# Kernel tuning notes

Hardware: AMD Instinct MI355X
Metric: run time of the kernel (lower is better)

Reference implementation:

```python
import jax, jax.numpy as jnp
import numpy as np
from functools import partial

B, C, FD, H, W = 8, 256, 128, 64, 64
POSC = 34  # 32 learned pos channels + 2 raw meshgrid channels


def create_meshgrid(h, w):
    # kornia-style normalized grid in [-1, 1], returned as [1, 2, h, w] (x, y)
    xs = jnp.linspace(-1.0, 1.0, w, dtype=jnp.float32)
    ys = jnp.linspace(-1.0, 1.0, h, dtype=jnp.float32)
    gy, gx = jnp.meshgrid(ys, xs, indexing='ij')
    return jnp.stack([gx, gy], axis=0)[None]  # [1,2,h,w]


def conv1x1(x, w, b):
    return jnp.einsum('bchw,oc->bohw', x, w) + b[None, :, None, None]


def pos_gen(feat, pg_w1, pg_b1, pg_w2, pg_b2):
    # PosGen type=2 with detach: two 1x1 'mul' layers (conv + ReLU, no norm)
    b, c, h, w = feat.shape
    feat = jax.lax.stop_gradient(feat)
    pos = jnp.broadcast_to(create_meshgrid(h, w), (b, 2, h, w))
    inp = jnp.concatenate([pos + 1.0, feat], axis=1)           # [b, feat_dim+2, h, w]
    h1 = jax.nn.relu(conv1x1(inp, pg_w1, pg_b1))               # [b, feat_dim, h, w]
    h2 = jax.nn.relu(conv1x1(h1, pg_w2, pg_b2))                # [b, 32, h, w]
    return jnp.concatenate([h2, pos], axis=1)                  # [b, 34, h, w]


def fuser(x, feat, w1, b1, w2, b2):
    # fuser_1D: concat along channels, 1x1 -> hidden (ReLU) -> 1x1 -> 256
    z = jnp.concatenate([x, feat], axis=1)
    z = jax.nn.relu(conv1x1(z, w1, b1))
    return conv1x1(z, w2, b2)


def conv_y(y, dw_w, dw_b, pw_w, pw_b):
    # BasicDWLayer: depthwise 3x3 + pointwise 1x1, no norm, no activation
    z = jax.lax.conv_general_dilated(
        y, dw_w, window_strides=(1, 1), padding='SAME',
        feature_group_count=y.shape[1],
        dimension_numbers=('NCHW', 'OIHW', 'NCHW')) + dw_b[None, :, None, None]
    return conv1x1(z, pw_w, pw_b)


def matching_forward(x, y, feat1, feat2,
                     pg_w1, pg_b1, pg_w2, pg_b2,
                     fus_w1, fus_b1, fus_w2, fus_b2,
                     dw_w, dw_b, pw_w, pw_b,
                     dustbin_vec, dustbin_pos):
    b, c, hx, wx = x.shape
    hy, wy = y.shape[2], y.shape[3]

    posf = pos_gen(feat2, pg_w1, pg_b1, pg_w2, pg_b2)          # [b, 34, hy, wy]
    c_pose = posf.shape[1]
    pos = posf.reshape(b, 1, c_pose, hy * wy).swapaxes(-1, -2)  # [b,1,Nk,34]

    xf = fuser(x, feat1, fus_w1, fus_b1, fus_w2, fus_b2)
    yf = fuser(y, feat2, fus_w1, fus_b1, fus_w2, fus_b2)
    yf = conv_y(yf, dw_w, dw_b, pw_w, pw_b)
    d = yf.shape[1]

    q = xf.reshape(b, 1, d, hx * wx).swapaxes(-1, -2)           # [b,1,Nq,256]
    k = yf.reshape(b, 1, d, hy * wy).swapaxes(-1, -2)           # [b,1,Nk,256]

    # dustbin token augmentation
    k = jnp.concatenate([k, jnp.broadcast_to(dustbin_vec, (b, 1, 1, d))], axis=-2)
    pos = jnp.concatenate([pos, jnp.broadcast_to(dustbin_pos, (b, 1, 1, c_pose))], axis=-2)

    # single-head cross-attention: values are the positional channels
    scores = jnp.einsum('bhqc,bhkc->bhqk', q, k) / jnp.sqrt(jnp.float32(d))
    attn = jax.nn.softmax(scores, axis=-1)
    out = jnp.einsum('bhqk,bhkd->bhqd', attn, pos)              # [b,1,Nq,34]
    return out.swapaxes(-1, -2).reshape(b, c_pose, hx, wx)


def setup_inputs() -> dict:
    key = jax.random.key(0)
    ks = jax.random.split(key, 20)
    s = 0.05
    return {
        'x': jax.random.normal(ks[0], (B, C, H, W), jnp.float32),
        'y': jax.random.normal(ks[1], (B, C, H, W), jnp.float32),
        'feat1': jax.random.normal(ks[2], (B, FD, H, W), jnp.float32),
        'feat2': jax.random.normal(ks[3], (B, FD, H, W), jnp.float32),
        # PosGen type-2 mapping: (feat_dim+2)->feat_dim, feat_dim->(hidden-2=32)
        'pg_w1': jax.random.normal(ks[4], (FD, FD + 2), jnp.float32) * s,
        'pg_b1': jnp.zeros((FD,), jnp.float32),
        'pg_w2': jax.random.normal(ks[5], (32, FD), jnp.float32) * s,
        'pg_b2': jnp.zeros((32,), jnp.float32),
        # fuser_1D: (256+128)->256 hidden, hidden->256
        'fus_w1': jax.random.normal(ks[6], (256, C + FD), jnp.float32) * s,
        'fus_b1': jnp.zeros((256,), jnp.float32),
        'fus_w2': jax.random.normal(ks[7], (C, 256), jnp.float32) * s,
        'fus_b2': jnp.zeros((C,), jnp.float32),
        # conv_y: depthwise 3x3 + pointwise 1x1
        'dw_w': jax.random.normal(ks[8], (C, 1, 3, 3), jnp.float32) * s,
        'dw_b': jnp.zeros((C,), jnp.float32),
        'pw_w': jax.random.normal(ks[9], (C, C), jnp.float32) * s,
        'pw_b': jnp.zeros((C,), jnp.float32),
        'dustbin_vec': jax.random.uniform(ks[10], (1, 1, 1, C), jnp.float32) / 10.0,
        'dustbin_pos': jnp.zeros((1, 1, 1, POSC), jnp.float32) - 10.0,
    }


def reference(x, y, feat1, feat2,
              pg_w1, pg_b1, pg_w2, pg_b2,
              fus_w1, fus_b1, fus_w2, fus_b2,
              dw_w, dw_b, pw_w, pw_b,
              dustbin_vec, dustbin_pos):
    return matching_forward(x, y, feat1, feat2,
                            pg_w1, pg_b1, pg_w2, pg_b2,
                            fus_w1, fus_b1, fus_w2, fus_b2,
                            dw_w, dw_b, pw_w, pw_b,
                            dustbin_vec, dustbin_pos)
```

## Files before the change

### kernel.cpp

```cpp
#include <hip/hip_runtime.h>
#include <hip/hip_bf16.h>

typedef __hip_bfloat16 bf16;
typedef unsigned short ushort_t;
typedef __bf16 bf16x8 __attribute__((ext_vector_type(8)));
typedef float  f32x4  __attribute__((ext_vector_type(4)));

#define HW    4096
#define NB    8
#define KSTR  4160
#define NTOK  32768
#define PROWS 64
#define QSCALE 0.0901684400557f

__device__ __forceinline__ float lde(const void* p, size_t i, int f32f) {
    return f32f ? ((const float*)p)[i] : (float)((const bf16*)p)[i];
}
__device__ __forceinline__ ushort_t f2bu(float f){ union { __bf16 b; ushort_t u; } cv; cv.b = (__bf16)f; return cv.u; }

__device__ __forceinline__ void async_cp16(const void* g, void* l) {
    __builtin_amdgcn_global_load_lds(
        (const __attribute__((address_space(1))) unsigned int*)g,
        (__attribute__((address_space(3))) unsigned int*)l, 16, 0, 0);
}

__global__ void detect_kernel(const ushort_t* xb, int* flag)
{
    __shared__ int cnt;
    const int t = threadIdx.x;
    if (t == 0) cnt = 0;
    __syncthreads();
    ushort_t h = xb[2*t];
    int e = (h >> 7) & 0xFF;
    if (e >= 133) atomicAdd(&cnt, 1);
    __syncthreads();
    if (t == 0) *flag = (cnt > 8) ? 1 : 0;
}

struct WsPtrs {
    bf16 *fw1t, *fw2t, *pwt, *pgw1t, *pgw2t, *dwt, *pos;
    float *posw, *fb1, *fb2, *pwb, *pgb1, *pgb2, *dwb;
};

__global__ __launch_bounds__(256) void prep_kernel(
    const void* fus_w1, const void* fus_w2, const void* pw_w,
    const void* pg_w1, const void* pg_w2, const void* dw_w,
    const void* fus_b1, const void* fus_b2, const void* pw_b,
    const void* pg_b1, const void* pg_b2, const void* dw_b,
    const void* dpos, WsPtrs W, const int* flag)
{
    const int f = *flag;
    const long n_w1 = 98304, n_w2 = 65536, n_pw = 65536, n_g1 = 16384, n_g2 = 4096;
    const long n_posw = 256, n_dwt = 2304;
    const long n_b = 256, n_gb1 = 128, n_gb2 = 32;
    const long n_mesh = 65536;
    const long n_pad  = 8L*14*KSTR;
    const long n_dust = 272;
    const long n_zt   = 8L*34*63;
    const long total = n_w1+n_w2+n_pw+n_g1+n_g2+n_posw+n_dwt
                     + 3*n_b + n_gb1 + n_gb2 + n_b + n_mesh + n_pad + n_dust + n_zt;

    for (long i = blockIdx.x*256L + threadIdx.x; i < total; i += gridDim.x*256L) {
        long j = i;
        if (j < n_w1) { W.fw1t[j] = __float2bfloat16(lde(fus_w1, j, f)); continue; } j -= n_w1;
        if (j < n_w2) { W.fw2t[j] = __float2bfloat16(lde(fus_w2, j, f)); continue; } j -= n_w2;
        if (j < n_pw) { W.pwt[j]  = __float2bfloat16(lde(pw_w,  j, f)); continue; } j -= n_pw;
        if (j < n_g1) { W.pgw1t[j] = __float2bfloat16(lde(pg_w1, (j>>7)*130 + 2 + (j&127), f)); continue; } j -= n_g1;
        if (j < n_g2) { W.pgw2t[j] = __float2bfloat16(lde(pg_w2, j, f)); continue; } j -= n_g2;
        if (j < n_posw) { W.posw[j] = lde(pg_w1, (j>>1)*130 + (j&1), f); continue; } j -= n_posw;
        if (j < n_dwt) { W.dwt[j] = __float2bfloat16(lde(dw_w, (j&255)*9 + (j>>8), f)); continue; } j -= n_dwt;
        if (j < n_b)   { W.fb1[j] = lde(fus_b1, j, f); continue; } j -= n_b;
        if (j < n_b)   { W.fb2[j] = lde(fus_b2, j, f); continue; } j -= n_b;
        if (j < n_b)   { W.pwb[j] = lde(pw_b, j, f); continue; } j -= n_b;
        if (j < n_gb1) { W.pgb1[j] = lde(pg_b1, j, f); continue; } j -= n_gb1;
        if (j < n_gb2) { W.pgb2[j] = lde(pg_b2, j, f); continue; } j -= n_gb2;
        if (j < n_b)   { W.dwb[j] = lde(dw_b, j, f); continue; } j -= n_b;
        if (j < n_mesh) {
            long b = j >> 13; int rr = (int)((j>>12)&1); int tok = (int)(j & 4095);
            float v = rr ? (-1.f + 2.f*(float)((tok>>6)&63)/63.f)
                         : (-1.f + 2.f*(float)(tok&63)/63.f);
            W.pos[((size_t)b*PROWS + 32 + rr)*KSTR + tok] = __float2bfloat16(v);
            continue;
        } j -= n_mesh;
        if (j < n_pad) {
            long b = j / (14L*KSTR); long rem = j % (14L*KSTR);
            int row = 34 + (int)(rem / KSTR); int tok = (int)(rem % KSTR);
            W.pos[((size_t)b*PROWS + row)*KSTR + tok] = __float2bfloat16(row == 34 ? 1.f : 0.f);
            continue;
        } j -= n_pad;
        if (j < n_dust) {
            long b = j / 34; int ch = (int)(j % 34);
            W.pos[((size_t)b*PROWS + ch)*KSTR + 4096] = __float2bfloat16(lde(dpos, ch, f));
            continue;
        } j -= n_dust;
        { long b = j / (34*63); long rem = j % (34*63);
          int ch = (int)(rem / 63); int cc = (int)(rem % 63);
          W.pos[((size_t)b*PROWS + ch)*KSTR + 4097 + cc] = __float2bfloat16(0.f); }
    }
}

__global__ __launch_bounds__(256) void transpose_kernel(
    const void* main_src, const void* feat_src, bf16* __restrict__ dst, const int* flag)
{
    __shared__ float Tt[64*65];
    const int t = threadIdx.x;
    const int p0 = blockIdx.x * 64;
    const int cht = blockIdx.y;
    const int b = blockIdx.z;
    const int f = *flag;

    const void* src; int ch0, srcC, dc0;
    if (cht < 4) { src = main_src; ch0 = cht*64; srcC = 256; dc0 = ch0; }
    else         { src = feat_src; ch0 = (cht-4)*64; srcC = 128; dc0 = 256 + (cht-4)*64; }

    const int p = t & 63, cq = t >> 6;
    #pragma unroll
    for (int e = 0; e < 16; ++e) {
        int c = e*4 + cq;
        Tt[p*65 + c] = lde(src, ((size_t)b*srcC + ch0 + c)*HW + p0 + p, f);
    }
    __syncthreads();
    const int pr = t >> 2, cs = (t & 3) * 16;
    union { uint4 u4[2]; ushort_t us[16]; } pk;
    #pragma unroll
    for (int u = 0; u < 16; ++u) pk.us[u] = f2bu(Tt[pr*65 + cs + u]);
    ushort_t* op = (ushort_t*)dst + ((size_t)b*HW + p0 + pr)*384 + dc0 + cs;
    *(uint4*)op = pk.u4[0];
    *((uint4*)op + 1) = pk.u4[1];
}

template<int MT, bool RELU, bool POSEPI, int OMODE>
__global__ __launch_bounds__(256) void gemm_mfma(
    const bf16* __restrict__ A, int sa,
    const bf16* __restrict__ Bw, int ldb,
    const float* __restrict__ bias, const float* __restrict__ posw,
    bf16* __restrict__ out, int sm, int K, float oscale)
{
    const int t = threadIdx.x;
    const int w = t >> 6, lane = t & 63;
    const int n = lane & 15, quad = lane >> 4;
    const int p0 = blockIdx.x * 128;
    const int m0 = blockIdx.y * (MT*16);
    const int rowbase = p0 + w*32;

    f32x4 acc[2][MT];
    #pragma unroll
    for (int pt = 0; pt < 2; ++pt)
        #pragma unroll
        for (int mt = 0; mt < MT; ++mt) acc[pt][mt] = (f32x4){0.f,0.f,0.f,0.f};

    for (int k0 = 0; k0 < K; k0 += 32) {
        bf16x8 ap[2];
        #pragma unroll
        for (int pt = 0; pt < 2; ++pt)
            ap[pt] = *(const bf16x8*)&A[(size_t)(rowbase + pt*16 + n)*sa + k0 + quad*8];
        #pragma unroll
        for (int mt = 0; mt < MT; ++mt) {
            bf16x8 bw = *(const bf16x8*)&Bw[(size_t)(m0 + mt*16 + n)*ldb + k0 + quad*8];
            acc[0][mt] = __builtin_amdgcn_mfma_f32_16x16x32_bf16(ap[0], bw, acc[0][mt], 0, 0, 0);
            acc[1][mt] = __builtin_amdgcn_mfma_f32_16x16x32_bf16(ap[1], bw, acc[1][mt], 0, 0, 0);
        }
    }

    #pragma unroll
    for (int mt = 0; mt < MT; ++mt) {
        const int m = m0 + mt*16 + n;
        const float bi = bias[m];
        float w0 = 0.f, w1 = 0.f;
        if (POSEPI) { w0 = posw[m*2]; w1 = posw[m*2 + 1]; }
        #pragma unroll
        for (int pt = 0; pt < 2; ++pt) {
            const int tokb = rowbase + pt*16 + quad*4;
            if (OMODE == 1) {
                union { uint2 u2; ushort_t us[4]; } pk;
                #pragma unroll
                for (int r = 0; r < 4; ++r) {
                    float v = acc[pt][mt][r] + bi;
                    if (RELU) v = fmaxf(v, 0.f);
                    pk.us[r] = f2bu(v * oscale);
                }
                size_t oi = ((size_t)(tokb >> 12)*PROWS + m)*KSTR + (tokb & 4095);
                *(uint2*)((ushort_t*)out + oi) = pk.u2;
            } else {
                #pragma unroll
                for (int r = 0; r < 4; ++r) {
                    int tok = tokb + r;
                    float v = acc[pt][mt][r] + bi;
                    if (POSEPI) {
                        float gx1 = 2.f * (float)(tok & 63) / 63.f;
                        float gy1 = 2.f * (float)((tok >> 6) & 63) / 63.f;
                        v += w0*gx1 + w1*gy1;
                    }
                    if (RELU) v = fmaxf(v, 0.f);
                    v *= oscale;
                    size_t row = (OMODE == 2) ? (size_t)tok + 64*(size_t)(tok >> 12) : (size_t)tok;
                    out[row*sm + m] = __float2bfloat16(v);
                }
            }
        }
    }
}

__global__ __launch_bounds__(256) void dw_kernel(
    const bf16* __restrict__ in, const bf16* __restrict__ dwt,
    const float* __restrict__ dwb, bf16* __restrict__ out)
{
    const int t = threadIdx.x;
    const int tok = blockIdx.x*8 + (t >> 5);
    const int c8 = (t & 31) * 8;
    const int b = tok >> 12, p = tok & 4095;
    const int i = p >> 6, j = p & 63;

    float acc[8];
    #pragma unroll
    for (int u = 0; u < 8; ++u) acc[u] = dwb[c8 + u];

    #pragma unroll
    for (int di = 0; di < 3; ++di) {
        int ii = i + di - 1;
        if (ii < 0 || ii >= 64) continue;
        #pragma unroll
        for (int dj = 0; dj < 3; ++dj) {
            int jj = j + dj - 1;
            if (jj < 0 || jj >= 64) continue;
            int tok2 = (b << 12) + ii*64 + jj;
            bf16x8 xv = *(const bf16x8*)&in[(size_t)tok2*256 + c8];
            bf16x8 wv = *(const bf16x8*)&dwt[(di*3 + dj)*256 + c8];
            #pragma unroll
            for (int u = 0; u < 8; ++u) acc[u] += (float)xv[u] * (float)wv[u];
        }
    }
    union { uint4 u4; ushort_t us[8]; } pk;
    #pragma unroll
    for (int u = 0; u < 8; ++u) pk.us[u] = f2bu(acc[u]);
    *(uint4*)((ushort_t*)out + (size_t)tok*256 + c8) = pk.u4;
}

__global__ __launch_bounds__(256) void fill_late_kernel(
    const void* dvec, bf16* __restrict__ k_t, const int* flag)
{
    const int b = blockIdx.x, t = threadIdx.x;
    k_t[((size_t)b*KSTR + 4096)*256 + t] = __float2bfloat16(lde(dvec, t, *flag));
}

__global__ __launch_bounds__(512, 2) void attn_kernel(
    const bf16* __restrict__ q_t, const bf16* __restrict__ k_t,
    const bf16* __restrict__ pos, void* outv, const int* flag)
{
    __shared__ __align__(16) __bf16 Ks[2*2048*8];
    __shared__ __align__(16) __bf16 posb[2*512*8];
    __shared__ __align__(16) __bf16 Pb[2*64*72];

    const int t = threadIdx.x;
    const int w = t >> 6, lane = t & 63;
    const int n = lane & 15, quad = lane >> 4;
    const int qg = w >> 2, ks = w & 3;
    const int bid = blockIdx.x;
    const int b = bid & 7;
    const int qt = bid >> 3;

    bf16x8 aq[4][8];
    #pragma unroll
    for (int f = 0; f < 4; ++f) {
        size_t qrow = (size_t)b*HW + qt*128 + qg*64 + f*16 + n;
        #pragma unroll
        for (int c = 0; c < 8; ++c)
            aq[f][c] = *(const bf16x8*)&q_t[qrow*256 + c*32 + quad*8];
    }

    f32x4 pacc[3];
    #pragma unroll
    for (int ct = 0; ct < 3; ++ct) pacc[ct] = (f32x4){0.f,0.f,0.f,0.f};

    const ushort_t* ksrc0 = (const ushort_t*)k_t + (size_t)b*KSTR*256;
    const ushort_t* psrc0 = (const ushort_t*)pos + (size_t)b*PROWS*KSTR;
    const int xw = n & 7;

    auto STAGE = [&](int kt2, int bufn) {
        const int kb = kt2 * 64;
        __bf16* kd = &Ks[(size_t)bufn*16384];
        #pragma unroll
        for (int e = 0; e < 4; ++e) {
            int slot = w*256 + e*64 + lane;
            int tok = slot >> 5;
            int ch = ((slot & 31) ^ (tok & 7)) * 8;
            async_cp16(&ksrc0[(size_t)(kb + tok)*256 + ch], &kd[(size_t)slot*8]);
        }
        {
            int slot = w*64 + lane;
            int row = slot >> 3;
            int ch = ((slot & 7) ^ (row & 7)) * 8;
            async_cp16(&psrc0[(size_t)row*KSTR + kb + ch], &posb[(size_t)(bufn*512 + slot)*8]);
        }
    };

    STAGE(0, 0);
    for (int kt = 0; kt < 65; ++kt) {
        const int cur = kt & 1;
        asm volatile("s_waitcnt vmcnt(0)" ::: "memory");
        __builtin_amdgcn_s_barrier();
        asm volatile("" ::: "memory");
        if (kt + 1 < 65) STAGE(kt + 1, cur ^ 1);

        const __bf16* kb_ = &Ks[(size_t)cur*16384];
        const __bf16* pb_ = &posb[(size_t)cur*4096];
        __bf16* Pq = &Pb[(size_t)qg*(64*72)];

        f32x4 sacc[4];
        #pragma unroll
        for (int f = 0; f < 4; ++f) sacc[f] = (f32x4){0.f,0.f,0.f,0.f};
        #pragma unroll
        for (int c = 0; c < 8; ++c) {
            bf16x8 bk = *(const bf16x8*)&kb_[(size_t)((ks*16 + n)*32 + ((c*4 + quad) ^ xw))*8];
            #pragma unroll
            for (int f = 0; f < 4; ++f)
                sacc[f] = __builtin_amdgcn_mfma_f32_16x16x32_bf16(aq[f][c], bk, sacc[f], 0, 0, 0);
        }

        const bool ok = (kt*64 + ks*16 + n) <= 4096;
        #pragma unroll
        for (int f = 0; f < 4; ++f)
            #pragma unroll
            for (int r = 0; r < 4; ++r) {
                float pv = ok ? __builtin_amdgcn_exp2f(sacc[f][r]) : 0.f;
                Pq[(f*16 + quad*4 + r)*72 + ks*16 + n] = (__bf16)pv;
            }

        asm volatile("s_waitcnt lgkmcnt(0)" ::: "memory");
        __builtin_amdgcn_s_barrier();
        asm volatile("" ::: "memory");

        #pragma unroll
        for (int c = 0; c < 2; ++c) {
            bf16x8 aP = *(const bf16x8*)&Pq[(size_t)((ks*16 + n)*72 + c*32 + quad*8)];
            #pragma unroll
            for (int ct = 0; ct < 3; ++ct) {
                bf16x8 bp = *(const bf16x8*)&pb_[(size_t)((ct*16 + n)*8 + ((c*4 + quad) ^ xw))*8];
                pacc[ct] = __builtin_amdgcn_mfma_f32_16x16x32_bf16(aP, bp, pacc[ct], 0, 0, 0);
            }
        }
    }
    asm volatile("s_waitcnt vmcnt(0)" ::: "memory");

    const int f32o = *flag;
    float linv[4];
    #pragma unroll
    for (int r = 0; r < 4; ++r)
        linv[r] = 1.f / __shfl(pacc[2][r], (lane & 48) | 2, 64);
    #pragma unroll
    for (int ct = 0; ct < 3; ++ct) {
        int ch = ct*16 + n;
        if (ch >= 34) continue;
        #pragma unroll
        for (int r = 0; r < 4; ++r) {
            float v = pacc[ct][r] * linv[r];
            size_t oi = ((size_t)b*34 + ch)*HW + qt*128 + qg*64 + ks*16 + quad*4 + r;
            if (f32o) ((float*)outv)[oi] = v;
            else      ((bf16*)outv)[oi]  = __float2bfloat16(v);
        }
    }
}

extern "C" void kernel_launch(void* const* d_in, const int* in_sizes, int n_in,
                              void* d_out, int out_size, void* d_ws, size_t ws_size,
                              hipStream_t stream)
{
    const void* x      = d_in[0];
    const void* y      = d_in[1];
    const void* feat1  = d_in[2];
    const void* feat2  = d_in[3];
    const void* pg_w1  = d_in[4];
    const void* pg_b1  = d_in[5];
    const void* pg_w2  = d_in[6];
    const void* pg_b2  = d_in[7];
    const void* fus_w1 = d_in[8];
    const void* fus_b1 = d_in[9];
    const void* fus_w2 = d_in[10];
    const void* fus_b2 = d_in[11];
    const void* dw_w   = d_in[12];
    const void* dw_b   = d_in[13];
    const void* pw_w   = d_in[14];
    const void* pw_b   = d_in[15];
    const void* dvec   = d_in[16];
    const void* dpos   = d_in[17];

    char* wsb = (char*)d_ws;
    int*  flag = (int*)wsb;
    size_t off = 16;
    bf16* R1   = (bf16*)(wsb + off); off += (size_t)NTOK*384*2;
    bf16* bufH = (bf16*)(wsb + off); off += (size_t)NTOK*256*2;
    bf16* q_t  = (bf16*)(wsb + off); off += (size_t)NTOK*256*2;
    bf16* pos  = (bf16*)(wsb + off); off += (size_t)NB*PROWS*KSTR*2;
    WsPtrs W;
    W.fw1t  = (bf16*)(wsb + off); off += 98304*2;
    W.fw2t  = (bf16*)(wsb + off); off += 65536*2;
    W.pwt   = (bf16*)(wsb + off); off += 65536*2;
    W.pgw1t = (bf16*)(wsb + off); off += 16384*2;
    W.pgw2t = (bf16*)(wsb + off); off += 4096*2;
    W.dwt   = (bf16*)(wsb + off); off += 2304*2;
    W.pos   = pos;
    W.posw  = (float*)(wsb + off); off += 256*4;
    W.fb1   = (float*)(wsb + off); off += 256*4;
    W.fb2   = (float*)(wsb + off); off += 256*4;
    W.pwb   = (float*)(wsb + off); off += 256*4;
    W.pgb1  = (float*)(wsb + off); off += 128*4;
    W.pgb2  = (float*)(wsb + off); off += 32*4;
    W.dwb   = (float*)(wsb + off); off += 256*4;

    bf16* in_xy = R1;
    bf16* yf    = R1;
    bf16* k_t   = R1;

    dim3 b256(256);

    detect_kernel<<<1, 256, 0, stream>>>((const ushort_t*)x, flag);
    prep_kernel<<<1024, b256, 0, stream>>>(fus_w1, fus_w2, pw_w, pg_w1, pg_w2, dw_w,
                                           fus_b1, fus_b2, pw_b, pg_b1, pg_b2, dw_b,
                                           dpos, W, flag);
    transpose_kernel<<<dim3(64,6,NB), b256, 0, stream>>>(x, feat1, in_xy, flag);
    gemm_mfma<8, true, false, 0><<<dim3(256,2), b256, 0, stream>>>(
        in_xy, 384, W.fw1t, 384, W.fb1, nullptr, bufH, 256, 384, 1.f);
    gemm_mfma<8, false, false, 0><<<dim3(256,2), b256, 0, stream>>>(
        bufH, 256, W.fw2t, 256, W.fb2, nullptr, q_t, 256, 256, QSCALE);
    transpose_kernel<<<dim3(64,6,NB), b256, 0, stream>>>(y, feat2, in_xy, flag);
    gemm_mfma<8, true, true, 0><<<dim3(256,1), b256, 0, stream>>>(
        in_xy + 256, 384, W.pgw1t, 128, W.pgb1, W.posw, bufH, 128, 128, 1.f);
    gemm_mfma<2, true, false, 1><<<dim3(256,1), b256, 0, stream>>>(
        bufH, 128, W.pgw2t, 128, W.pgb2, nullptr, pos, 0, 128, 1.f);
    gemm_mfma<8, true, false, 0><<<dim3(256,2), b256, 0, stream>>>(
        in_xy, 384, W.fw1t, 384, W.fb1, nullptr, bufH, 256, 384, 1.f);
    gemm_mfma<8, false, false, 0><<<dim3(256,2), b256, 0, stream>>>(
        bufH, 256, W.fw2t, 256, W.fb2, nullptr, yf, 256, 256, 1.f);
    dw_kernel<<<dim3(4096), b256, 0, stream>>>(yf, W.dwt, W.dwb, bufH);
    fill_late_kernel<<<dim3(NB), b256, 0, stream>>>(dvec, k_t, flag);
    gemm_mfma<8, false, false, 2><<<dim3(256,2), b256, 0, stream>>>(
        bufH, 256, W.pwt, 256, W.pwb, nullptr, k_t, 256, 256, 1.f);
    attn_kernel<<<dim3(256), dim3(512), 0, stream>>>(q_t, k_t, pos, d_out, flag);
}
```

Before: 499.0 us.

## Halve attention query tile, swap MFMA operands, reuse K buffer for P

The attention kernel now uses 256-thread blocks over 64 queries each, with 512 blocks instead of 256 blocks of 512 threads. The score MFMA operands are swapped so each lane holds four consecutive keys and can pack P into a single 8-byte store. P is written into the current K LDS buffer after the QK pass, which removes the separate P buffer and shrinks the pos buffer to 48 rows. This cuts LDS use and doubles the grid for occupancy and load balance. The cost is that each K tile is loaded twice as often per query and each block issues twice the async copies.

Result: faster. 480.2 us (-3.8%).

```diff
diff --git a/kernel.cpp b/kernel.cpp
--- a/kernel.cpp
+++ b/kernel.cpp
@@ -243,29 +243,29 @@
     k_t[((size_t)b*KSTR + 4096)*256 + t] = __float2bfloat16(lde(dvec, t, *flag));
 }
 
-__global__ __launch_bounds__(512, 2) void attn_kernel(
+__global__ __launch_bounds__(256, 2) void attn_kernel(
     const bf16* __restrict__ q_t, const bf16* __restrict__ k_t,
     const bf16* __restrict__ pos, void* outv, const int* flag)
 {
-    __shared__ __align__(16) __bf16 Ks[2*2048*8];
-    __shared__ __align__(16) __bf16 posb[2*512*8];
-    __shared__ __align__(16) __bf16 Pb[2*64*72];
+    __shared__ __align__(16) __bf16 Ks[2*16384];
+    __shared__ __align__(16) __bf16 posb[2*3072];
 
     const int t = threadIdx.x;
     const int w = t >> 6, lane = t & 63;
     const int n = lane & 15, quad = lane >> 4;
-    const int qg = w >> 2, ks = w & 3;
     const int bid = blockIdx.x;
     const int b = bid & 7;
     const int qt = bid >> 3;
+    const int ks = w;
+    const int xw = n & 7;
 
     bf16x8 aq[4][8];
     #pragma unroll
-    for (int f = 0; f < 4; ++f) {
-        size_t qrow = (size_t)b*HW + qt*128 + qg*64 + f*16 + n;
+    for (int qf = 0; qf < 4; ++qf) {
+        size_t qrow = (size_t)b*HW + qt*64 + qf*16 + n;
         #pragma unroll
         for (int c = 0; c < 8; ++c)
-            aq[f][c] = *(const bf16x8*)&q_t[qrow*256 + c*32 + quad*8];
+            aq[qf][c] = *(const bf16x8*)&q_t[qrow*256 + c*32 + quad*8];
     }
 
     f32x4 pacc[3];
@@ -274,23 +274,25 @@
 
     const ushort_t* ksrc0 = (const ushort_t*)k_t + (size_t)b*KSTR*256;
     const ushort_t* psrc0 = (const ushort_t*)pos + (size_t)b*PROWS*KSTR;
-    const int xw = n & 7;
 
     auto STAGE = [&](int kt2, int bufn) {
         const int kb = kt2 * 64;
         __bf16* kd = &Ks[(size_t)bufn*16384];
         #pragma unroll
-        for (int e = 0; e < 4; ++e) {
-            int slot = w*256 + e*64 + lane;
+        for (int e = 0; e < 8; ++e) {
+            int slot = w*512 + e*64 + lane;
             int tok = slot >> 5;
             int ch = ((slot & 31) ^ (tok & 7)) * 8;
             async_cp16(&ksrc0[(size_t)(kb + tok)*256 + ch], &kd[(size_t)slot*8]);
         }
-        {
-            int slot = w*64 + lane;
-            int row = slot >> 3;
-            int ch = ((slot & 7) ^ (row & 7)) * 8;
-            async_cp16(&psrc0[(size_t)row*KSTR + kb + ch], &posb[(size_t)(bufn*512 + slot)*8]);
+        if (w < 3) {
+            #pragma unroll
+            for (int e = 0; e < 2; ++e) {
+                int slot = w*128 + e*64 + lane;
+                int row = slot >> 3;
+                int ch = ((slot & 7) ^ (row & 7)) * 8;
+                async_cp16(&psrc0[(size_t)row*KSTR + kb + ch], &posb[(size_t)(bufn*3072 + slot*8)]);
+            }
         }
     };
 
@@ -302,29 +304,31 @@
         asm volatile("" ::: "memory");
         if (kt + 1 < 65) STAGE(kt + 1, cur ^ 1);
 
-        const __bf16* kb_ = &Ks[(size_t)cur*16384];
-        const __bf16* pb_ = &posb[(size_t)cur*4096];
-        __bf16* Pq = &Pb[(size_t)qg*(64*72)];
+        __bf16* kb_ = &Ks[(size_t)cur*16384];
+        const __bf16* pb_ = &posb[(size_t)cur*3072];
 
         f32x4 sacc[4];
         #pragma unroll
-        for (int f = 0; f < 4; ++f) sacc[f] = (f32x4){0.f,0.f,0.f,0.f};
+        for (int qf = 0; qf < 4; ++qf) sacc[qf] = (f32x4){0.f,0.f,0.f,0.f};
         #pragma unroll
         for (int c = 0; c < 8; ++c) {
             bf16x8 bk = *(const bf16x8*)&kb_[(size_t)((ks*16 + n)*32 + ((c*4 + quad) ^ xw))*8];
             #pragma unroll
-            for (int f = 0; f < 4; ++f)
-                sacc[f] = __builtin_amdgcn_mfma_f32_16x16x32_bf16(aq[f][c], bk, sacc[f], 0, 0, 0);
-        }
-
-        const bool ok = (kt*64 + ks*16 + n) <= 4096;
-        #pragma unroll
-        for (int f = 0; f < 4; ++f)
+            for (int qf = 0; qf < 4; ++qf)
+                sacc[qf] = __builtin_amdgcn_mfma_f32_16x16x32_bf16(bk, aq[qf][c], sacc[qf], 0, 0, 0);
+        }
+
+        const int tokb = kt*64 + ks*16 + quad*4;
+        #pragma unroll
+        for (int qf = 0; qf < 4; ++qf) {
+            union { uint2 u2; ushort_t us[4]; } pk;
             #pragma unroll
             for (int r = 0; r < 4; ++r) {
-                float pv = ok ? __builtin_amdgcn_exp2f(sacc[f][r]) : 0.f;
-                Pq[(f*16 + quad*4 + r)*72 + ks*16 + n] = (__bf16)pv;
+                float e = __builtin_amdgcn_exp2f(sacc[qf][r]);
+                pk.us[r] = f2bu((tokb + r <= 4096) ? e : 0.f);
             }
+            *(uint2*)&kb_[(size_t)ks*4096 + (qf*16 + n)*16 + quad*4] = pk.u2;
+        }
 
         asm volatile("s_waitcnt lgkmcnt(0)" ::: "memory");
         __builtin_amdgcn_s_barrier();
@@ -332,7 +336,8 @@
 
         #pragma unroll
         for (int c = 0; c < 2; ++c) {
-            bf16x8 aP = *(const bf16x8*)&Pq[(size_t)((ks*16 + n)*72 + c*32 + quad*8)];
+            int s = c*2 + (quad >> 1);
+            bf16x8 aP = *(const bf16x8*)&kb_[(size_t)s*4096 + (w*16 + n)*16 + (quad & 1)*8];
             #pragma unroll
             for (int ct = 0; ct < 3; ++ct) {
                 bf16x8 bp = *(const bf16x8*)&pb_[(size_t)((ct*16 + n)*8 + ((c*4 + quad) ^ xw))*8];
@@ -340,7 +345,6 @@
             }
         }
     }
-    asm volatile("s_waitcnt vmcnt(0)" ::: "memory");
 
     const int f32o = *flag;
     float linv[4];
@@ -354,7 +358,7 @@
         #pragma unroll
         for (int r = 0; r < 4; ++r) {
             float v = pacc[ct][r] * linv[r];
-            size_t oi = ((size_t)b*34 + ch)*HW + qt*128 + qg*64 + ks*16 + quad*4 + r;
+            size_t oi = ((size_t)b*34 + ch)*HW + qt*64 + w*16 + quad*4 + r;
             if (f32o) ((float*)outv)[oi] = v;
             else      ((bf16*)outv)[oi]  = __float2bfloat16(v);
         }
@@ -435,5 +439,5 @@
     fill_late_kernel<<<dim3(NB), b256, 0, stream>>>(dvec, k_t, flag);
     gemm_mfma<8, false, false, 2><<<dim3(256,2), b256, 0, stream>>>(
         bufH, 256, W.pwt, 256, W.pwb, nullptr, k_t, 256, 256, 1.f);
-    attn_kernel<<<dim3(256), dim3(512), 0, stream>>>(q_t, k_t, pos, d_out, flag);
-}
+    attn_kernel<<<dim3(512), b256, 0, stream>>>(q_t, k_t, pos, d_out, flag);
+}
```
